# Kernel optimization log

Hardware: AMD Instinct MI355X
Metric: run time of the kernel (lower is better)

## Reference

```python
import jax, jax.numpy as jnp
import numpy as np

# FFT-based (Makhoul) inverse DCT-II along the last axis.
#   y_n = X_0/2 + sum_{k=1}^{N-1} X_k * cos(pi*k*(2n+1)/(2N))
# expk is the complex twiddle exp(1j*pi*k/(2N)), k = 0..N-1.

def _idct_last(X, expk):
    N = X.shape[-1]
    # X_{N-k} with the k=0 slot set to 0
    Xr = jnp.concatenate([jnp.zeros_like(X[..., :1]), jnp.flip(X[..., 1:], axis=-1)], axis=-1)
    V = 0.5 * (X - 1j * Xr) * expk              # half-spectrum with twiddles
    v = jnp.fft.ifft(V, axis=-1).real * N        # undo jnp.fft's 1/N
    h = N // 2                                   # N assumed even (grid dims are)
    # de-interleave: y_{2m} = v_m, y_{2m+1} = v_{N-1-m}
    y = jnp.stack([v[..., :h], jnp.flip(v, axis=-1)[..., :h]], axis=-1)
    return y.reshape(X.shape)


def _idxst_last(X, expk):
    # y_n = sum_{k=1}^{N-1} X_k * sin(pi*k*(2n+1)/(2N))
    #     = (-1)^n * IDCT(X')_n  with X'_k = X_{N-k}, X'_0 = 0
    N = X.shape[-1]
    Xf = jnp.concatenate([jnp.zeros_like(X[..., :1]), jnp.flip(X[..., 1:], axis=-1)], axis=-1)
    sign = jnp.where(jnp.arange(N) % 2 == 0, 1.0, -1.0).astype(X.dtype)
    return sign * _idct_last(Xf, expk)


def setup_inputs() -> dict:
    key = jax.random.key(0)
    B, M, N = 2, 4096, 4096
    x = jax.random.normal(key, (B, M, N), dtype=jnp.float32)

    def make_expk(K):
        k = np.arange(K, dtype=np.float64)
        ang = np.pi * k / (2.0 * K)
        return jnp.asarray(np.stack([np.cos(ang), np.sin(ang)], axis=-1), dtype=jnp.float32)

    return {"x": x, "expkM": make_expk(M), "expkN": make_expk(N)}


def reference(x, expkM, expkN):
    ekM = expkM[:, 0] + 1j * expkM[:, 1]   # exp(1j*pi*k/(2M))
    ekN = expkN[:, 0] + 1j * expkN[:, 1]   # exp(1j*pi*k/(2N))
    # IDCT along the M (row) dimension: move it to last axis
    y = _idct_last(jnp.swapaxes(x, -1, -2), ekM)
    y = jnp.swapaxes(y, -1, -2)
    # IDXST along the N (column) dimension
    return _idxst_last(y, ekN)
```

## Files before the change

### kernel.cpp

```cpp
#include <hip/hip_runtime.h>

#define PI_F 3.14159265358979323846f

__device__ __forceinline__ float2 cmulf(float2 a, float c, float s) {
    return make_float2(a.x * c - a.y * s, a.x * s + a.y * c);
}

#define SW(e) ((e) ^ ((((e) >> 4) & 3) * 5))

template<bool IDXST>
__global__ __launch_bounds__(512, 8)
void row_fft_kernel(const float* __restrict__ in, float* __restrict__ out,
                    const float2* __restrict__ expk)
{
    __shared__ float smem[8192];
    float*  xs   = smem;
    float2* bufB = (float2*)smem;
    float2* bufA = (float2*)(smem + 4096);

    const int t = threadIdx.x;
    const size_t row = blockIdx.x;
    const float* src = in  + row * 4096;
    float*       dst = out + row * 4096;

    {
        const float4* s4 = (const float4*)src;
        float4* x4 = (float4*)xs;
        x4[t]       = s4[t];
        x4[t + 512] = s4[t + 512];
    }
    __syncthreads();

    float2 z[4];
    #pragma unroll
    for (int i = 0; i < 4; i++) {
        int k = t + 512 * i;
        float Xa, Xra, Xb, Xrb;
        if (IDXST) {
            Xa  = xs[(4096 - k) & 4095];
            Xra = xs[k];
            Xb  = xs[2048 - k];
            Xrb = xs[2048 + k];
            if (k == 0) { Xa = 0.0f; Xra = 0.0f; }
        } else {
            Xa  = xs[k];
            Xra = xs[(4096 - k) & 4095];
            Xb  = xs[2048 + k];
            Xrb = xs[2048 - k];
            if (k == 0) Xra = 0.0f;
        }
        float2 ea = expk[k];
        float2 eb = expk[k + 2048];
        float Var = 0.5f * (Xa * ea.x + Xra * ea.y);
        float Vai = 0.5f * (Xa * ea.y - Xra * ea.x);
        float Vbr = 0.5f * (Xb * eb.x + Xrb * eb.y);
        float Vbi = 0.5f * (Xb * eb.y - Xrb * eb.x);
        float Ar = Var + Vbr, Ai = Vai + Vbi;
        float Dr = Var - Vbr, Di = Vai - Vbi;
        float cw, sw;
        __sincosf(PI_F * (float)k * (1.0f / 2048.0f), &sw, &cw);
        float Br = Dr * cw - Di * sw;
        float Bi = Dr * sw + Di * cw;
        z[i] = make_float2(Ar - Bi, Ai + Br);
    }

    {
        float2 v0 = z[0], v1 = z[1], v2 = z[2], v3 = z[3];
        float a0r = v0.x + v2.x, a0i = v0.y + v2.y;
        float a1r = v0.x - v2.x, a1i = v0.y - v2.y;
        float a2r = v1.x + v3.x, a2i = v1.y + v3.y;
        float a3r = v1.x - v3.x, a3i = v1.y - v3.y;
        int e = t << 2;
        bufA[SW(e)]     = make_float2(a0r + a2r, a0i + a2i);
        bufA[SW(e + 1)] = make_float2(a1r - a3i, a1i + a3r);
        bufA[SW(e + 2)] = make_float2(a0r - a2r, a0i - a2i);
        bufA[SW(e + 3)] = make_float2(a1r + a3i, a1i - a3r);
    }
    __syncthreads();

    float2* sb = bufA;
    float2* db = bufB;
    int Ns = 4;
    #pragma unroll
    for (int s = 1; s < 5; s++) {
        const int ls = 2 * s;
        const int j = t;
        float2 v0 = sb[SW(j)];
        float2 v1 = sb[SW(j + 512)];
        float2 v2 = sb[SW(j + 1024)];
        float2 v3 = sb[SW(j + 1536)];
        int jm = j & (Ns - 1);
        float c1, s1;
        if (s <= 2) {
            float2 e1 = expk[jm << (12 - 2 * s)];
            c1 = e1.x; s1 = e1.y;
        } else {
            __sincosf((0.5f * PI_F) * (float)jm / (float)Ns, &s1, &c1);
        }
        float c2 = c1 * c1 - s1 * s1, s2 = 2.0f * c1 * s1;
        float c3 = c1 * c2 - s1 * s2, s3 = c1 * s2 + s1 * c2;
        v1 = cmulf(v1, c1, s1);
        v2 = cmulf(v2, c2, s2);
        v3 = cmulf(v3, c3, s3);
        float a0r = v0.x + v2.x, a0i = v0.y + v2.y;
        float a1r = v0.x - v2.x, a1i = v0.y - v2.y;
        float a2r = v1.x + v3.x, a2i = v1.y + v3.y;
        float a3r = v1.x - v3.x, a3i = v1.y - v3.y;
        int idxD = ((j >> ls) << (ls + 2)) | jm;
        db[SW(idxD)]          = make_float2(a0r + a2r, a0i + a2i);
        db[SW(idxD + Ns)]     = make_float2(a1r - a3i, a1i + a3r);
        db[SW(idxD + 2 * Ns)] = make_float2(a0r - a2r, a0i - a2i);
        db[SW(idxD + 3 * Ns)] = make_float2(a1r + a3i, a1i - a3r);
        __syncthreads();
        float2* tmp = sb; sb = db; db = tmp;
        Ns <<= 2;
    }

    {
        int j  = t;
        int jB = 1023 - t;
        float2 a0 = sb[SW(j)];
        float2 a1 = sb[SW(j + 1024)];
        float2 b0 = sb[SW(jB)];
        float2 b1 = sb[SW(jB + 1024)];
        float sA, cA, sB, cB;
        __sincosf(PI_F * (float)j  * (1.0f / 1024.0f), &sA, &cA);
        __sincosf(PI_F * (float)jB * (1.0f / 1024.0f), &sB, &cB);
        float2 wa1 = cmulf(a1, cA, sA);
        float2 wb1 = cmulf(b1, cB, sB);
        float2 zA0 = make_float2(a0.x + wa1.x, a0.y + wa1.y);
        float2 zA1 = make_float2(a0.x - wa1.x, a0.y - wa1.y);
        float2 zB0 = make_float2(b0.x + wb1.x, b0.y + wb1.y);
        float2 zB1 = make_float2(b0.x - wb1.x, b0.y - wb1.y);
        float4 oA, oB;
        if (IDXST) {
            oA = make_float4(zA0.x, -zB1.y, zA0.y, -zB1.x);
            oB = make_float4(zB0.x, -zA1.y, zB0.y, -zA1.x);
        } else {
            oA = make_float4(zA0.x,  zB1.y, zA0.y,  zB1.x);
            oB = make_float4(zB0.x,  zA1.y, zB0.y,  zA1.x);
        }
        float4* d4 = (float4*)dst;
        d4[j]  = oA;
        d4[jB] = oB;
    }
}

__global__ __launch_bounds__(256)
void transpose_inplace(float* d, int n)
{
    __shared__ float ta[64][65];
    __shared__ float tb[64][65];
    int ti = blockIdx.x, tj = blockIdx.y, b = blockIdx.z;
    if (tj < ti) return;
    float* base = d + (size_t)b * n * n;
    const int t  = threadIdx.x;
    const int c4 = t & 15;
    const int r0 = t >> 4;
    size_t offA = (size_t)(ti * 64) * n + tj * 64;
    size_t offB = (size_t)(tj * 64) * n + ti * 64;

    #pragma unroll
    for (int q = 0; q < 4; q++) {
        int r = r0 + 16 * q;
        float4 va = ((const float4*)(base + offA + (size_t)r * n))[c4];
        ta[r][4 * c4 + 0] = va.x; ta[r][4 * c4 + 1] = va.y;
        ta[r][4 * c4 + 2] = va.z; ta[r][4 * c4 + 3] = va.w;
    }
    if (ti != tj) {
        #pragma unroll
        for (int q = 0; q < 4; q++) {
            int r = r0 + 16 * q;
            float4 vb = ((const float4*)(base + offB + (size_t)r * n))[c4];
            tb[r][4 * c4 + 0] = vb.x; tb[r][4 * c4 + 1] = vb.y;
            tb[r][4 * c4 + 2] = vb.z; tb[r][4 * c4 + 3] = vb.w;
        }
    }
    __syncthreads();

    if (ti != tj) {
        #pragma unroll
        for (int q = 0; q < 4; q++) {
            int r = r0 + 16 * q;
            float4 o;
            o.x = tb[4 * c4 + 0][r]; o.y = tb[4 * c4 + 1][r];
            o.z = tb[4 * c4 + 2][r]; o.w = tb[4 * c4 + 3][r];
            ((float4*)(base + offA + (size_t)r * n))[c4] = o;
            float4 p;
            p.x = ta[4 * c4 + 0][r]; p.y = ta[4 * c4 + 1][r];
            p.z = ta[4 * c4 + 2][r]; p.w = ta[4 * c4 + 3][r];
            ((float4*)(base + offB + (size_t)r * n))[c4] = p;
        }
    } else {
        #pragma unroll
        for (int q = 0; q < 4; q++) {
            int r = r0 + 16 * q;
            float4 p;
            p.x = ta[4 * c4 + 0][r]; p.y = ta[4 * c4 + 1][r];
            p.z = ta[4 * c4 + 2][r]; p.w = ta[4 * c4 + 3][r];
            ((float4*)(base + offA + (size_t)r * n))[c4] = p;
        }
    }
}

extern "C" void kernel_launch(void* const* d_in, const int* in_sizes, int n_in,
                              void* d_out, int out_size, void* d_ws, size_t ws_size,
                              hipStream_t stream)
{
    const float*  x     = (const float*)d_in[0];
    const float2* expkM = (const float2*)d_in[1];
    const float2* expkN = (const float2*)d_in[2];
    float* out = (float*)d_out;

    const int B = in_sizes[0] / (4096 * 4096);
    const int rows = B * 4096;

    row_fft_kernel<true><<<rows, 512, 0, stream>>>(x, out, expkN);
    transpose_inplace<<<dim3(64, 64, B), dim3(256), 0, stream>>>(out, 4096);
    row_fft_kernel<false><<<rows, 512, 0, stream>>>(out, out, expkM);
    transpose_inplace<<<dim3(64, 64, B), dim3(256), 0, stream>>>(out, 4096);
}
```

Before: 368.9 us.

## Replace transpose-FFT-transpose with two-pass strided column FFT via workspace

The M-axis IDCT no longer transposes in place, runs the row FFT and transposes back. It now uses two column-wise kernels that do a 64×32 decomposed FFT directly on strided columns, with an intermediate twiddled buffer held in the workspace. This cuts the global memory passes from three read-write round trips to two. The cost is very large per-thread register arrays and a small grid, which may limit occupancy and latency hiding. The old path is kept as a fallback when the workspace is too small.

New measurement: 587.7 us. 59.3% more time.

```diff
diff --git a/kernel.cpp b/kernel.cpp
--- a/kernel.cpp
+++ b/kernel.cpp
@@ -5,6 +5,18 @@
 __device__ __forceinline__ float2 cmulf(float2 a, float c, float s) {
     return make_float2(a.x * c - a.y * s, a.x * s + a.y * c);
 }
+
+#define BFLY4(v0, v1, v2, v3, o0, o1, o2, o3)                                  \
+    {                                                                          \
+        float a0r = v0.x + v2.x, a0i = v0.y + v2.y;                            \
+        float a1r = v0.x - v2.x, a1i = v0.y - v2.y;                            \
+        float a2r = v1.x + v3.x, a2i = v1.y + v3.y;                            \
+        float a3r = v1.x - v3.x, a3i = v1.y - v3.y;                            \
+        o0 = make_float2(a0r + a2r, a0i + a2i);                                \
+        o1 = make_float2(a1r - a3i, a1i + a3r);                                \
+        o2 = make_float2(a0r - a2r, a0i - a2i);                                \
+        o3 = make_float2(a1r + a3i, a1i - a3r);                                \
+    }
 
 #define SW(e) ((e) ^ ((((e) >> 4) & 3) * 5))
 
@@ -66,15 +78,9 @@
 
     {
         float2 v0 = z[0], v1 = z[1], v2 = z[2], v3 = z[3];
-        float a0r = v0.x + v2.x, a0i = v0.y + v2.y;
-        float a1r = v0.x - v2.x, a1i = v0.y - v2.y;
-        float a2r = v1.x + v3.x, a2i = v1.y + v3.y;
-        float a3r = v1.x - v3.x, a3i = v1.y - v3.y;
         int e = t << 2;
-        bufA[SW(e)]     = make_float2(a0r + a2r, a0i + a2i);
-        bufA[SW(e + 1)] = make_float2(a1r - a3i, a1i + a3r);
-        bufA[SW(e + 2)] = make_float2(a0r - a2r, a0i - a2i);
-        bufA[SW(e + 3)] = make_float2(a1r + a3i, a1i - a3r);
+        BFLY4(v0, v1, v2, v3,
+              bufA[SW(e)], bufA[SW(e + 1)], bufA[SW(e + 2)], bufA[SW(e + 3)]);
     }
     __syncthreads();
 
@@ -102,15 +108,10 @@
         v1 = cmulf(v1, c1, s1);
         v2 = cmulf(v2, c2, s2);
         v3 = cmulf(v3, c3, s3);
-        float a0r = v0.x + v2.x, a0i = v0.y + v2.y;
-        float a1r = v0.x - v2.x, a1i = v0.y - v2.y;
-        float a2r = v1.x + v3.x, a2i = v1.y + v3.y;
-        float a3r = v1.x - v3.x, a3i = v1.y - v3.y;
         int idxD = ((j >> ls) << (ls + 2)) | jm;
-        db[SW(idxD)]          = make_float2(a0r + a2r, a0i + a2i);
-        db[SW(idxD + Ns)]     = make_float2(a1r - a3i, a1i + a3r);
-        db[SW(idxD + 2 * Ns)] = make_float2(a0r - a2r, a0i - a2i);
-        db[SW(idxD + 3 * Ns)] = make_float2(a1r + a3i, a1i - a3r);
+        BFLY4(v0, v1, v2, v3,
+              db[SW(idxD)], db[SW(idxD + Ns)],
+              db[SW(idxD + 2 * Ns)], db[SW(idxD + 3 * Ns)]);
         __syncthreads();
         float2* tmp = sb; sb = db; db = tmp;
         Ns <<= 2;
@@ -146,6 +147,150 @@
     }
 }
 
+
+__global__ __launch_bounds__(256)
+void col_pass1(const float* __restrict__ g, float2* __restrict__ w,
+               const float2* __restrict__ expk)
+{
+    const int col = blockIdx.x * 64 + threadIdx.x;
+    const int m2  = blockIdx.y * 4 + threadIdx.y;
+    const float* G = g + (size_t)blockIdx.z * 4096 * 4096;
+    float2*      W = w + (size_t)blockIdx.z * 2048 * 4096;
+
+    float2 za[64], zb[64];
+
+    #pragma unroll
+    for (int m1 = 0; m1 < 64; m1++) {
+        int k = 32 * m1 + m2;
+        float Xa  = G[(size_t)k * 4096 + col];
+        float Xra = (k == 0) ? 0.0f : G[(size_t)(4096 - k) * 4096 + col];
+        float Xb  = G[(size_t)(2048 + k) * 4096 + col];
+        float Xrb = G[(size_t)(2048 - k) * 4096 + col];
+        float2 ea = expk[k];
+        float2 eb = expk[k + 2048];
+        float Var = 0.5f * (Xa * ea.x + Xra * ea.y);
+        float Vai = 0.5f * (Xa * ea.y - Xra * ea.x);
+        float Vbr = 0.5f * (Xb * eb.x + Xrb * eb.y);
+        float Vbi = 0.5f * (Xb * eb.y - Xrb * eb.x);
+        float Ar = Var + Vbr, Ai = Vai + Vbi;
+        float Dr = Var - Vbr, Di = Vai - Vbi;
+        float cw, sw;
+        __sincosf(PI_F * (float)k * (1.0f / 2048.0f), &sw, &cw);
+        float Br = Dr * cw - Di * sw;
+        float Bi = Dr * sw + Di * cw;
+        za[m1] = make_float2(Ar - Bi, Ai + Br);
+    }
+
+    #pragma unroll
+    for (int j = 0; j < 16; j++) {
+        float2 v0 = za[j], v1 = za[j + 16], v2 = za[j + 32], v3 = za[j + 48];
+        BFLY4(v0, v1, v2, v3, zb[4 * j], zb[4 * j + 1], zb[4 * j + 2], zb[4 * j + 3]);
+    }
+    #pragma unroll
+    for (int j = 0; j < 16; j++) {
+        float2 v0 = zb[j], v1 = zb[j + 16], v2 = zb[j + 32], v3 = zb[j + 48];
+        int jm = j & 3;
+        float s1, c1;
+        __sincosf((2.0f * PI_F / 16.0f) * (float)jm, &s1, &c1);
+        float c2 = c1 * c1 - s1 * s1, s2 = 2.0f * c1 * s1;
+        float c3 = c1 * c2 - s1 * s2, s3 = c1 * s2 + s1 * c2;
+        v1 = cmulf(v1, c1, s1);
+        v2 = cmulf(v2, c2, s2);
+        v3 = cmulf(v3, c3, s3);
+        int d = ((j >> 2) << 4) | jm;
+        BFLY4(v0, v1, v2, v3, za[d], za[d + 4], za[d + 8], za[d + 12]);
+    }
+    #pragma unroll
+    for (int j = 0; j < 16; j++) {
+        float2 v0 = za[j], v1 = za[j + 16], v2 = za[j + 32], v3 = za[j + 48];
+        float s1, c1;
+        __sincosf((2.0f * PI_F / 64.0f) * (float)j, &s1, &c1);
+        float c2 = c1 * c1 - s1 * s1, s2 = 2.0f * c1 * s1;
+        float c3 = c1 * c2 - s1 * s2, s3 = c1 * s2 + s1 * c2;
+        v1 = cmulf(v1, c1, s1);
+        v2 = cmulf(v2, c2, s2);
+        v3 = cmulf(v3, c3, s3);
+        BFLY4(v0, v1, v2, v3, zb[j], zb[j + 16], zb[j + 32], zb[j + 48]);
+    }
+
+    const float theta = (2.0f * PI_F / 2048.0f) * (float)m2;
+    #pragma unroll
+    for (int m1p = 0; m1p < 64; m1p++) {
+        float st, ct;
+        __sincosf(theta * (float)m1p, &st, &ct);
+        W[(size_t)(32 * m1p + m2) * 4096 + col] = cmulf(zb[m1p], ct, st);
+    }
+}
+
+__global__ __launch_bounds__(256)
+void col_pass2(const float2* __restrict__ w, float* __restrict__ y)
+{
+    const int col = blockIdx.x * 64 + threadIdx.x;
+    const int p   = blockIdx.y * 4 + threadIdx.y;
+    const int pb  = 63 - p;
+    const float2* W = w + (size_t)blockIdx.z * 2048 * 4096;
+    float*        Y = y + (size_t)blockIdx.z * 4096 * 4096;
+
+    float2 va[32], wa[32], vb[32], wb[32];
+    #pragma unroll
+    for (int m2 = 0; m2 < 32; m2++) {
+        va[m2] = W[(size_t)(32 * p  + m2) * 4096 + col];
+        vb[m2] = W[(size_t)(32 * pb + m2) * 4096 + col];
+    }
+
+    #pragma unroll
+    for (int j = 0; j < 8; j++) {
+        float2 v0 = va[j], v1 = va[j + 8], v2 = va[j + 16], v3 = va[j + 24];
+        BFLY4(v0, v1, v2, v3, wa[4 * j], wa[4 * j + 1], wa[4 * j + 2], wa[4 * j + 3]);
+        float2 u0 = vb[j], u1 = vb[j + 8], u2 = vb[j + 16], u3 = vb[j + 24];
+        BFLY4(u0, u1, u2, u3, wb[4 * j], wb[4 * j + 1], wb[4 * j + 2], wb[4 * j + 3]);
+    }
+    #pragma unroll
+    for (int j = 0; j < 8; j++) {
+        int jm = j & 3;
+        float s1, c1;
+        __sincosf((2.0f * PI_F / 16.0f) * (float)jm, &s1, &c1);
+        float c2 = c1 * c1 - s1 * s1, s2 = 2.0f * c1 * s1;
+        float c3 = c1 * c2 - s1 * s2, s3 = c1 * s2 + s1 * c2;
+        int d = ((j >> 2) << 4) | jm;
+        float2 v0 = wa[j], v1 = wa[j + 8], v2 = wa[j + 16], v3 = wa[j + 24];
+        v1 = cmulf(v1, c1, s1); v2 = cmulf(v2, c2, s2); v3 = cmulf(v3, c3, s3);
+        BFLY4(v0, v1, v2, v3, va[d], va[d + 4], va[d + 8], va[d + 12]);
+        float2 u0 = wb[j], u1 = wb[j + 8], u2 = wb[j + 16], u3 = wb[j + 24];
+        u1 = cmulf(u1, c1, s1); u2 = cmulf(u2, c2, s2); u3 = cmulf(u3, c3, s3);
+        BFLY4(u0, u1, u2, u3, vb[d], vb[d + 4], vb[d + 8], vb[d + 12]);
+    }
+    #pragma unroll
+    for (int j = 0; j < 16; j++) {
+        float s1, c1;
+        __sincosf((2.0f * PI_F / 32.0f) * (float)j, &s1, &c1);
+        float2 tA = cmulf(va[j + 16], c1, s1);
+        wa[j]      = make_float2(va[j].x + tA.x, va[j].y + tA.y);
+        wa[j + 16] = make_float2(va[j].x - tA.x, va[j].y - tA.y);
+        float2 tB = cmulf(vb[j + 16], c1, s1);
+        wb[j]      = make_float2(vb[j].x + tB.x, vb[j].y + tB.y);
+        wb[j + 16] = make_float2(vb[j].x - tB.x, vb[j].y - tB.y);
+    }
+
+    #pragma unroll
+    for (int q = 0; q < 16; q++) {
+        int p1 = p  + 64 * q;
+        int p2 = pb + 64 * q;
+        float2 z1  = wa[q];
+        float2 z1m = wb[31 - q];
+        float2 z2  = wb[q];
+        float2 z2m = wa[31 - q];
+        Y[(size_t)(4 * p1 + 0) * 4096 + col] = z1.x;
+        Y[(size_t)(4 * p1 + 1) * 4096 + col] = z1m.y;
+        Y[(size_t)(4 * p1 + 2) * 4096 + col] = z1.y;
+        Y[(size_t)(4 * p1 + 3) * 4096 + col] = z1m.x;
+        Y[(size_t)(4 * p2 + 0) * 4096 + col] = z2.x;
+        Y[(size_t)(4 * p2 + 1) * 4096 + col] = z2m.y;
+        Y[(size_t)(4 * p2 + 2) * 4096 + col] = z2.y;
+        Y[(size_t)(4 * p2 + 3) * 4096 + col] = z2m.x;
+    }
+}
+
 __global__ __launch_bounds__(256)
 void transpose_inplace(float* d, int n)
 {
@@ -186,19 +331,19 @@
             o.x = tb[4 * c4 + 0][r]; o.y = tb[4 * c4 + 1][r];
             o.z = tb[4 * c4 + 2][r]; o.w = tb[4 * c4 + 3][r];
             ((float4*)(base + offA + (size_t)r * n))[c4] = o;
-            float4 p;
-            p.x = ta[4 * c4 + 0][r]; p.y = ta[4 * c4 + 1][r];
-            p.z = ta[4 * c4 + 2][r]; p.w = ta[4 * c4 + 3][r];
-            ((float4*)(base + offB + (size_t)r * n))[c4] = p;
+            float4 pp;
+            pp.x = ta[4 * c4 + 0][r]; pp.y = ta[4 * c4 + 1][r];
+            pp.z = ta[4 * c4 + 2][r]; pp.w = ta[4 * c4 + 3][r];
+            ((float4*)(base + offB + (size_t)r * n))[c4] = pp;
         }
     } else {
         #pragma unroll
         for (int q = 0; q < 4; q++) {
             int r = r0 + 16 * q;
-            float4 p;
-            p.x = ta[4 * c4 + 0][r]; p.y = ta[4 * c4 + 1][r];
-            p.z = ta[4 * c4 + 2][r]; p.w = ta[4 * c4 + 3][r];
-            ((float4*)(base + offA + (size_t)r * n))[c4] = p;
+            float4 pp;
+            pp.x = ta[4 * c4 + 0][r]; pp.y = ta[4 * c4 + 1][r];
+            pp.z = ta[4 * c4 + 2][r]; pp.w = ta[4 * c4 + 3][r];
+            ((float4*)(base + offA + (size_t)r * n))[c4] = pp;
         }
     }
 }
@@ -216,7 +361,15 @@
     const int rows = B * 4096;
 
     row_fft_kernel<true><<<rows, 512, 0, stream>>>(x, out, expkN);
-    transpose_inplace<<<dim3(64, 64, B), dim3(256), 0, stream>>>(out, 4096);
-    row_fft_kernel<false><<<rows, 512, 0, stream>>>(out, out, expkM);
-    transpose_inplace<<<dim3(64, 64, B), dim3(256), 0, stream>>>(out, 4096);
-}
+
+    const size_t need = (size_t)B * 2048 * 4096 * sizeof(float2);
+    if (d_ws && ws_size >= need) {
+        float2* W = (float2*)d_ws;
+        col_pass1<<<dim3(64, 8, B), dim3(64, 4), 0, stream>>>(out, W, expkM);
+        col_pass2<<<dim3(64, 8, B), dim3(64, 4), 0, stream>>>(W, out);
+    } else {
+        transpose_inplace<<<dim3(64, 64, B), dim3(256), 0, stream>>>(out, 4096);
+        row_fft_kernel<false><<<rows, 512, 0, stream>>>(out, out, expkM);
+        transpose_inplace<<<dim3(64, 64, B), dim3(256), 0, stream>>>(out, 4096);
+    }
+}
```

## Replace transpose-FFT-transpose column IDCT with two-pass strided column FFT

Applied to the files above, without the earlier changes.

The column-direction IDCT no longer transposes the matrix twice around a row FFT. It runs a four-step decomposition: the first pass builds the twiddled half-spectrum, applies radix-4/2 stages and writes a twiddled intermediate to workspace. The second pass finishes the FFT and writes de-interleaved output rows directly, working on column pairs with float4 accesses. This removes two full in-place transpose passes, but needs a workspace buffer and falls back to the old path when the workspace is missing or too small.

Result: faster. 338.8 us (-8.2%).

```diff
diff --git a/kernel.cpp b/kernel.cpp
--- a/kernel.cpp
+++ b/kernel.cpp
@@ -1,12 +1,67 @@
 #include <hip/hip_runtime.h>
 
 #define PI_F 3.14159265358979323846f
+#define RSQ2 0.70710678118654752f
 
 __device__ __forceinline__ float2 cmulf(float2 a, float c, float s) {
     return make_float2(a.x * c - a.y * s, a.x * s + a.y * c);
 }
 
+__device__ __forceinline__ float4 dadd(float4 a, float4 b) {
+    return make_float4(a.x + b.x, a.y + b.y, a.z + b.z, a.w + b.w);
+}
+__device__ __forceinline__ float4 dsub(float4 a, float4 b) {
+    return make_float4(a.x - b.x, a.y - b.y, a.z - b.z, a.w - b.w);
+}
+__device__ __forceinline__ float4 dmuli(float4 a) {
+    return make_float4(-a.y, a.x, -a.w, a.z);
+}
+__device__ __forceinline__ float4 dmul(float4 a, float c, float s) {
+    return make_float4(a.x * c - a.y * s, a.x * s + a.y * c,
+                       a.z * c - a.w * s, a.z * s + a.w * c);
+}
+__device__ __forceinline__ void dif4(float4& z0, float4& z1, float4& z2,
+                                     float4& z3, float c1, float s1) {
+    float4 t0 = dadd(z0, z2), t1 = dsub(z0, z2);
+    float4 t2 = dadd(z1, z3), t3 = dsub(z1, z3);
+    float c2 = c1 * c1 - s1 * s1, s2 = 2.0f * c1 * s1;
+    float c3 = c1 * c2 - s1 * s2, s3 = c1 * s2 + s1 * c2;
+    z0 = dadd(t0, t2);
+    z1 = dmul(dadd(t1, dmuli(t3)), c1, s1);
+    z2 = dmul(dsub(t0, t2), c2, s2);
+    z3 = dmul(dsub(t1, dmuli(t3)), c3, s3);
+}
+__device__ __forceinline__ void dif4nt(float4& z0, float4& z1, float4& z2,
+                                       float4& z3) {
+    float4 t0 = dadd(z0, z2), t1 = dsub(z0, z2);
+    float4 t2 = dadd(z1, z3), t3 = dsub(z1, z3);
+    z0 = dadd(t0, t2);
+    z1 = dadd(t1, dmuli(t3));
+    z2 = dsub(t0, t2);
+    z3 = dsub(t1, dmuli(t3));
+}
+__device__ __forceinline__ float2 quadrot(float2 e, int qd) {
+    switch (qd & 3) {
+        case 0:  return make_float2( e.x,  e.y);
+        case 1:  return make_float2(-e.y,  e.x);
+        case 2:  return make_float2(-e.x, -e.y);
+        default: return make_float2( e.y, -e.x);
+    }
+}
+
 #define SW(e) ((e) ^ ((((e) >> 4) & 3) * 5))
+
+#define BFLY4(v0, v1, v2, v3, o0, o1, o2, o3)                                  \
+    {                                                                          \
+        float a0r = v0.x + v2.x, a0i = v0.y + v2.y;                            \
+        float a1r = v0.x - v2.x, a1i = v0.y - v2.y;                            \
+        float a2r = v1.x + v3.x, a2i = v1.y + v3.y;                            \
+        float a3r = v1.x - v3.x, a3i = v1.y - v3.y;                            \
+        o0 = make_float2(a0r + a2r, a0i + a2i);                                \
+        o1 = make_float2(a1r - a3i, a1i + a3r);                                \
+        o2 = make_float2(a0r - a2r, a0i - a2i);                                \
+        o3 = make_float2(a1r + a3i, a1i - a3r);                                \
+    }
 
 template<bool IDXST>
 __global__ __launch_bounds__(512, 8)
@@ -66,15 +121,9 @@
 
     {
         float2 v0 = z[0], v1 = z[1], v2 = z[2], v3 = z[3];
-        float a0r = v0.x + v2.x, a0i = v0.y + v2.y;
-        float a1r = v0.x - v2.x, a1i = v0.y - v2.y;
-        float a2r = v1.x + v3.x, a2i = v1.y + v3.y;
-        float a3r = v1.x - v3.x, a3i = v1.y - v3.y;
         int e = t << 2;
-        bufA[SW(e)]     = make_float2(a0r + a2r, a0i + a2i);
-        bufA[SW(e + 1)] = make_float2(a1r - a3i, a1i + a3r);
-        bufA[SW(e + 2)] = make_float2(a0r - a2r, a0i - a2i);
-        bufA[SW(e + 3)] = make_float2(a1r + a3i, a1i - a3r);
+        BFLY4(v0, v1, v2, v3,
+              bufA[SW(e)], bufA[SW(e + 1)], bufA[SW(e + 2)], bufA[SW(e + 3)]);
     }
     __syncthreads();
 
@@ -102,15 +151,10 @@
         v1 = cmulf(v1, c1, s1);
         v2 = cmulf(v2, c2, s2);
         v3 = cmulf(v3, c3, s3);
-        float a0r = v0.x + v2.x, a0i = v0.y + v2.y;
-        float a1r = v0.x - v2.x, a1i = v0.y - v2.y;
-        float a2r = v1.x + v3.x, a2i = v1.y + v3.y;
-        float a3r = v1.x - v3.x, a3i = v1.y - v3.y;
         int idxD = ((j >> ls) << (ls + 2)) | jm;
-        db[SW(idxD)]          = make_float2(a0r + a2r, a0i + a2i);
-        db[SW(idxD + Ns)]     = make_float2(a1r - a3i, a1i + a3r);
-        db[SW(idxD + 2 * Ns)] = make_float2(a0r - a2r, a0i - a2i);
-        db[SW(idxD + 3 * Ns)] = make_float2(a1r + a3i, a1i - a3r);
+        BFLY4(v0, v1, v2, v3,
+              db[SW(idxD)], db[SW(idxD + Ns)],
+              db[SW(idxD + 2 * Ns)], db[SW(idxD + 3 * Ns)]);
         __syncthreads();
         float2* tmp = sb; sb = db; db = tmp;
         Ns <<= 2;
@@ -146,6 +190,206 @@
     }
 }
 
+
+__device__ __forceinline__ float2 zb1(float Xa, float Xra, float Xb, float Xrb,
+                                      float2 ea, float2 eb, float cw, float sw) {
+    float Var = 0.5f * (Xa * ea.x + Xra * ea.y);
+    float Vai = 0.5f * (Xa * ea.y - Xra * ea.x);
+    float Vbr = 0.5f * (Xb * eb.x + Xrb * eb.y);
+    float Vbi = 0.5f * (Xb * eb.y - Xrb * eb.x);
+    float Ar = Var + Vbr, Ai = Vai + Vbi;
+    float Dr = Var - Vbr, Di = Vai - Vbi;
+    float Br = Dr * cw - Di * sw;
+    float Bi = Dr * sw + Di * cw;
+    return make_float2(Ar - Bi, Ai + Br);
+}
+
+__device__ __forceinline__ float4 zbuild(const float* __restrict__ G,
+                                         const float2* __restrict__ expk,
+                                         int m1, int m2, int colf, float2 u) {
+    int k = 64 * m1 + m2;
+    float2 Xa  = *(const float2*)&G[(size_t)k * 4096 + colf];
+    float2 Xra = make_float2(0.0f, 0.0f);
+    if (k != 0) Xra = *(const float2*)&G[(size_t)(4096 - k) * 4096 + colf];
+    float2 Xb  = *(const float2*)&G[(size_t)(2048 + k) * 4096 + colf];
+    float2 Xrb = *(const float2*)&G[(size_t)(2048 - k) * 4096 + colf];
+    float2 ea = expk[k];
+    float2 eb = expk[k + 2048];
+    float2 ev = expk[256 * (m1 & 15)];
+    float vc = (m1 < 16) ? ev.x : -ev.y;
+    float vs = (m1 < 16) ? ev.y :  ev.x;
+    float cw = u.x * vc - u.y * vs;
+    float sw = u.x * vs + u.y * vc;
+    float2 lo = zb1(Xa.x, Xra.x, Xb.x, Xrb.x, ea, eb, cw, sw);
+    float2 hi = zb1(Xa.y, Xra.y, Xb.y, Xrb.y, ea, eb, cw, sw);
+    return make_float4(lo.x, lo.y, hi.x, hi.y);
+}
+
+__global__ __launch_bounds__(512, 4)
+void col_pass1(const float* __restrict__ g, float2* __restrict__ wbuf,
+               const float2* __restrict__ expk)
+{
+    __shared__ float4 zs[32 * 64];
+    const int c    = threadIdx.x;
+    const int gq   = threadIdx.y;
+    const int colf = 2 * (blockIdx.x * 64 + c);
+    const int m2   = blockIdx.y;
+    const float* G = g    + (size_t)blockIdx.z * 4096 * 4096;
+    float2*      W = wbuf + (size_t)blockIdx.z * 2048 * 4096;
+
+    const float2 u = expk[4 * m2];
+
+    float4 z0 = zbuild(G, expk, gq,      m2, colf, u);
+    float4 z1 = zbuild(G, expk, gq + 8,  m2, colf, u);
+    float4 z2 = zbuild(G, expk, gq + 16, m2, colf, u);
+    float4 z3 = zbuild(G, expk, gq + 24, m2, colf, u);
+
+    if (gq == 0) { dif4nt(z0, z1, z2, z3); }
+    else { float2 e1 = expk[512 * gq]; dif4(z0, z1, z2, z3, e1.x, e1.y); }
+    zs[(gq     ) * 64 + c] = z0;
+    zs[(gq +  8) * 64 + c] = z1;
+    zs[(gq + 16) * 64 + c] = z2;
+    zs[(gq + 24) * 64 + c] = z3;
+    __syncthreads();
+
+    {
+        int b = 8 * (gq >> 1), j = gq & 1;
+        float4 y0 = zs[(b + j    ) * 64 + c];
+        float4 y1 = zs[(b + j + 2) * 64 + c];
+        float4 y2 = zs[(b + j + 4) * 64 + c];
+        float4 y3 = zs[(b + j + 6) * 64 + c];
+        if (j == 0) { dif4nt(y0, y1, y2, y3); }
+        else        { dif4(y0, y1, y2, y3, RSQ2, RSQ2); }
+        zs[(b + j    ) * 64 + c] = y0;
+        zs[(b + j + 2) * 64 + c] = y1;
+        zs[(b + j + 4) * 64 + c] = y2;
+        zs[(b + j + 6) * 64 + c] = y3;
+    }
+    __syncthreads();
+
+    {
+        float4 w0 = zs[(4 * gq    ) * 64 + c];
+        float4 w1 = zs[(4 * gq + 1) * 64 + c];
+        float4 w2 = zs[(4 * gq + 2) * 64 + c];
+        float4 w3 = zs[(4 * gq + 3) * 64 + c];
+        float4 s0 = dadd(w0, w1), s1 = dsub(w0, w1);
+        float4 s2 = dadd(w2, w3), s3 = dsub(w2, w3);
+
+#define P1_STORE(v, p) {                                                       \
+        int n1_ = ((p) >> 3) + 4 * (((p) >> 1) & 3) + 16 * ((p) & 1);          \
+        int a_  = n1_ * m2;                                                    \
+        float2 tw = quadrot(expk[8 * (a_ & 511)], a_ >> 9);                    \
+        *(float4*)&W[(size_t)(64 * n1_ + m2) * 4096 + colf] =                  \
+            dmul(v, tw.x, tw.y); }
+        P1_STORE(s0, 4 * gq + 0);
+        P1_STORE(s1, 4 * gq + 1);
+        P1_STORE(s2, 4 * gq + 2);
+        P1_STORE(s3, 4 * gq + 3);
+#undef P1_STORE
+    }
+}
+
+__global__ __launch_bounds__(512, 4)
+void col_pass2(const float2* __restrict__ wbuf, float* __restrict__ y,
+               const float2* __restrict__ expk)
+{
+    __shared__ float4 zs[64 * 64];
+    const int c    = threadIdx.x;
+    const int gq   = threadIdx.y;
+    const int colf = 2 * (blockIdx.x * 64 + c);
+    const int n1   = blockIdx.y;
+    const float2* W = wbuf + (size_t)blockIdx.z * 2048 * 4096;
+    float*        Y = y    + (size_t)blockIdx.z * 4096 * 4096;
+
+    const int j0 = 2 * gq, j1 = 2 * gq + 1;
+
+    float4 a0 = *(const float4*)&W[(size_t)(64 * n1 + j0     ) * 4096 + colf];
+    float4 a1 = *(const float4*)&W[(size_t)(64 * n1 + j0 + 16) * 4096 + colf];
+    float4 a2 = *(const float4*)&W[(size_t)(64 * n1 + j0 + 32) * 4096 + colf];
+    float4 a3 = *(const float4*)&W[(size_t)(64 * n1 + j0 + 48) * 4096 + colf];
+    float4 b0 = *(const float4*)&W[(size_t)(64 * n1 + j1     ) * 4096 + colf];
+    float4 b1 = *(const float4*)&W[(size_t)(64 * n1 + j1 + 16) * 4096 + colf];
+    float4 b2 = *(const float4*)&W[(size_t)(64 * n1 + j1 + 32) * 4096 + colf];
+    float4 b3 = *(const float4*)&W[(size_t)(64 * n1 + j1 + 48) * 4096 + colf];
+
+    if (gq == 0) { dif4nt(a0, a1, a2, a3); }
+    else { float2 e1 = expk[256 * j0]; dif4(a0, a1, a2, a3, e1.x, e1.y); }
+    { float2 e1 = expk[256 * j1]; dif4(b0, b1, b2, b3, e1.x, e1.y); }
+    zs[(j0     ) * 64 + c] = a0;
+    zs[(j0 + 16) * 64 + c] = a1;
+    zs[(j0 + 32) * 64 + c] = a2;
+    zs[(j0 + 48) * 64 + c] = a3;
+    zs[(j1     ) * 64 + c] = b0;
+    zs[(j1 + 16) * 64 + c] = b1;
+    zs[(j1 + 32) * 64 + c] = b2;
+    zs[(j1 + 48) * 64 + c] = b3;
+    __syncthreads();
+
+    {
+        int bb = 16 * (j0 >> 2), jj = j0 & 3;
+        float4 y0 = zs[(bb + jj     ) * 64 + c];
+        float4 y1 = zs[(bb + jj +  4) * 64 + c];
+        float4 y2 = zs[(bb + jj +  8) * 64 + c];
+        float4 y3 = zs[(bb + jj + 12) * 64 + c];
+        if (jj == 0) { dif4nt(y0, y1, y2, y3); }
+        else { float2 e1 = expk[1024 * jj]; dif4(y0, y1, y2, y3, e1.x, e1.y); }
+        zs[(bb + jj     ) * 64 + c] = y0;
+        zs[(bb + jj +  4) * 64 + c] = y1;
+        zs[(bb + jj +  8) * 64 + c] = y2;
+        zs[(bb + jj + 12) * 64 + c] = y3;
+    }
+    {
+        int bb = 16 * (j1 >> 2), jj = j1 & 3;
+        float4 y0 = zs[(bb + jj     ) * 64 + c];
+        float4 y1 = zs[(bb + jj +  4) * 64 + c];
+        float4 y2 = zs[(bb + jj +  8) * 64 + c];
+        float4 y3 = zs[(bb + jj + 12) * 64 + c];
+        if (jj == 0) { dif4nt(y0, y1, y2, y3); }
+        else { float2 e1 = expk[1024 * jj]; dif4(y0, y1, y2, y3, e1.x, e1.y); }
+        zs[(bb + jj     ) * 64 + c] = y0;
+        zs[(bb + jj +  4) * 64 + c] = y1;
+        zs[(bb + jj +  8) * 64 + c] = y2;
+        zs[(bb + jj + 12) * 64 + c] = y3;
+    }
+    __syncthreads();
+
+    float4 w0 = zs[(8 * gq + 0) * 64 + c];
+    float4 w1 = zs[(8 * gq + 1) * 64 + c];
+    float4 w2 = zs[(8 * gq + 2) * 64 + c];
+    float4 w3 = zs[(8 * gq + 3) * 64 + c];
+    float4 w4 = zs[(8 * gq + 4) * 64 + c];
+    float4 w5 = zs[(8 * gq + 5) * 64 + c];
+    float4 w6 = zs[(8 * gq + 6) * 64 + c];
+    float4 w7 = zs[(8 * gq + 7) * 64 + c];
+    dif4nt(w0, w1, w2, w3);
+    dif4nt(w4, w5, w6, w7);
+
+#define P2_STORE(v, p) {                                                       \
+    int n2_ = ((p) >> 4) + ((p) & 12) + (((p) & 3) << 4);                      \
+    int q_  = n1 + 32 * n2_;                                                   \
+    if (((p) & 3) < 2) {                                                       \
+        *(float2*)&Y[(size_t)(4 * q_ + 0) * 4096 + colf] =                     \
+            make_float2(v.x, v.z);                                             \
+        *(float2*)&Y[(size_t)(4 * q_ + 2) * 4096 + colf] =                     \
+            make_float2(v.y, v.w);                                             \
+    } else {                                                                   \
+        int pp_ = 2047 - q_;                                                   \
+        *(float2*)&Y[(size_t)(4 * pp_ + 1) * 4096 + colf] =                    \
+            make_float2(v.y, v.w);                                             \
+        *(float2*)&Y[(size_t)(4 * pp_ + 3) * 4096 + colf] =                    \
+            make_float2(v.x, v.z);                                             \
+    } }
+    P2_STORE(w0, 8 * gq + 0);
+    P2_STORE(w1, 8 * gq + 1);
+    P2_STORE(w2, 8 * gq + 2);
+    P2_STORE(w3, 8 * gq + 3);
+    P2_STORE(w4, 8 * gq + 4);
+    P2_STORE(w5, 8 * gq + 5);
+    P2_STORE(w6, 8 * gq + 6);
+    P2_STORE(w7, 8 * gq + 7);
+#undef P2_STORE
+}
+
 __global__ __launch_bounds__(256)
 void transpose_inplace(float* d, int n)
 {
@@ -186,19 +430,19 @@
             o.x = tb[4 * c4 + 0][r]; o.y = tb[4 * c4 + 1][r];
             o.z = tb[4 * c4 + 2][r]; o.w = tb[4 * c4 + 3][r];
             ((float4*)(base + offA + (size_t)r * n))[c4] = o;
-            float4 p;
-            p.x = ta[4 * c4 + 0][r]; p.y = ta[4 * c4 + 1][r];
-            p.z = ta[4 * c4 + 2][r]; p.w = ta[4 * c4 + 3][r];
-            ((float4*)(base + offB + (size_t)r * n))[c4] = p;
+            float4 pp;
+            pp.x = ta[4 * c4 + 0][r]; pp.y = ta[4 * c4 + 1][r];
+            pp.z = ta[4 * c4 + 2][r]; pp.w = ta[4 * c4 + 3][r];
+            ((float4*)(base + offB + (size_t)r * n))[c4] = pp;
         }
     } else {
         #pragma unroll
         for (int q = 0; q < 4; q++) {
             int r = r0 + 16 * q;
-            float4 p;
-            p.x = ta[4 * c4 + 0][r]; p.y = ta[4 * c4 + 1][r];
-            p.z = ta[4 * c4 + 2][r]; p.w = ta[4 * c4 + 3][r];
-            ((float4*)(base + offA + (size_t)r * n))[c4] = p;
+            float4 pp;
+            pp.x = ta[4 * c4 + 0][r]; pp.y = ta[4 * c4 + 1][r];
+            pp.z = ta[4 * c4 + 2][r]; pp.w = ta[4 * c4 + 3][r];
+            ((float4*)(base + offA + (size_t)r * n))[c4] = pp;
         }
     }
 }
@@ -216,7 +460,15 @@
     const int rows = B * 4096;
 
     row_fft_kernel<true><<<rows, 512, 0, stream>>>(x, out, expkN);
-    transpose_inplace<<<dim3(64, 64, B), dim3(256), 0, stream>>>(out, 4096);
-    row_fft_kernel<false><<<rows, 512, 0, stream>>>(out, out, expkM);
-    transpose_inplace<<<dim3(64, 64, B), dim3(256), 0, stream>>>(out, 4096);
-}
+
+    const size_t need = (size_t)B * 2048 * 4096 * sizeof(float2);
+    if (d_ws && ws_size >= need) {
+        float2* W = (float2*)d_ws;
+        col_pass1<<<dim3(32, 64, B), dim3(64, 8), 0, stream>>>(out, W, expkM);
+        col_pass2<<<dim3(32, 32, B), dim3(64, 8), 0, stream>>>(W, out, expkM);
+    } else {
+        transpose_inplace<<<dim3(64, 64, B), dim3(256), 0, stream>>>(out, 4096);
+        row_fft_kernel<false><<<rows, 512, 0, stream>>>(out, out, expkM);
+        transpose_inplace<<<dim3(64, 64, B), dim3(256), 0, stream>>>(out, 4096);
+    }
+}
```
